# Performance work log

Hardware: AMD Instinct MI355X
Metric: run time of the kernel (lower is better)

The kernel has to match this reference:

```python
import jax, jax.numpy as jnp
import numpy as np

N, L = 64, 128
D = (32, 16, 8)   # input mode dims
H = (32, 16, 8)   # hidden mode dims


def setup_inputs() -> dict:
    key = jax.random.key(0)
    ks = jax.random.split(key, 7)
    inputs = jax.random.normal(ks[0], (N, L, *D), dtype=jnp.float32)
    # 3 gates (z, r, h) stacked along leading axis g; one factor matrix per mode.
    W1 = jax.random.normal(ks[1], (3, H[0], D[0]), dtype=jnp.float32) * 0.1
    W2 = jax.random.normal(ks[2], (3, H[1], D[1]), dtype=jnp.float32) * 0.1
    W3 = jax.random.normal(ks[3], (3, H[2], D[2]), dtype=jnp.float32) * 0.1
    U1 = jax.random.normal(ks[4], (3, H[0], H[0]), dtype=jnp.float32) * 0.1
    U2 = jax.random.normal(ks[5], (3, H[1], H[1]), dtype=jnp.float32) * 0.1
    U3 = jax.random.normal(ks[6], (3, H[2], H[2]), dtype=jnp.float32) * 0.1
    return {"inputs": inputs, "W1": W1, "W2": W2, "W3": W3,
            "U1": U1, "U2": U2, "U3": U3}


def reference(inputs, W1, W2, W3, U1, U2, U3):
    # batch_first -> (L, N, a, b, c)
    x = jnp.transpose(inputs, (1, 0, 2, 3, 4))
    # Precompute input projections for all timesteps and all 3 gates at once
    # (same math as applying TCL per step; mode-wise tensor contraction).
    XW = jnp.einsum('lnabc,gda,geb,gfc->lgndef', x, W1, W2, W3)  # (L,3,N,h1,h2,h3)
    h0 = jnp.zeros((x.shape[1], U1.shape[1], U2.shape[1], U3.shape[1]), x.dtype)

    def step(h, xw):
        hu = jnp.einsum('nabc,gda,geb,gfc->gndef', h, U1, U2, U3)  # (3,N,h1,h2,h3)
        z = jax.nn.sigmoid(xw[0] + hu[0])
        r = jax.nn.sigmoid(xw[1] + hu[1])
        hh = jnp.tanh(xw[2] + r * hu[2])
        h_new = z * h + (1.0 - z) * hh
        return h_new, h_new

    h_last, outs = jax.lax.scan(step, h0, XW)          # outs: (L,N,h1,h2,h3)
    outs = jnp.transpose(outs, (1, 0, 2, 3, 4))         # back to batch_first
    return outs, h_last
```

## Files before the change

### kernel.cpp

```cpp
#include <hip/hip_runtime.h>
#include <stdint.h>


constexpr int kN = 64;
constexpr int kL = 128;
constexpr int kA = 32, kB = 16, kC = 8;
constexpr int kBC = kB * kC;
constexpr int kTot = kA * kBC;
constexpr int kTS = kBC + 4;
constexpr int kTh = 512;
constexpr int kXwTiles = 8;

constexpr int kHTS = 40;
constexpr int kT1S = 136;

typedef __attribute__((ext_vector_type(8))) short bf16x8;
typedef __attribute__((ext_vector_type(4))) float f32x4;

namespace {

__device__ __forceinline__ float bf2f(unsigned int u) { return __uint_as_float(u << 16); }
__device__ __forceinline__ unsigned int f2bf(float v) {
  unsigned int u = __float_as_uint(v);
  return (u + 0x7fffu + ((u >> 16) & 1u)) >> 16;
}
__device__ __forceinline__ float sigmoid_f(float x) {
  return __fdividef(1.f, 1.f + __expf(-x));
}
__device__ __forceinline__ float tanh_f(float x) {
  return 1.f - __fdividef(2.f, 1.f + __expf(2.f * x));
}

__device__ __forceinline__ bf16x8 frag_from_lds(const unsigned short* p) {
  uint4 u = *(const uint4*)p;
  return __builtin_bit_cast(bf16x8, u);
}
__device__ __forceinline__ bf16x8 frag_from_f32(const float* p) {
  float4 a = ((const float4*)p)[0];
  float4 b = ((const float4*)p)[1];
  uint4 u;
  u.x = f2bf(a.x) | (f2bf(a.y) << 16);
  u.y = f2bf(a.z) | (f2bf(a.w) << 16);
  u.z = f2bf(b.x) | (f2bf(b.y) << 16);
  u.w = f2bf(b.z) | (f2bf(b.w) << 16);
  return __builtin_bit_cast(bf16x8, u);
}
__device__ __forceinline__ uint2 pack4(const f32x4& a) {
  uint2 p;
  p.x = f2bf(a[0]) | (f2bf(a[1]) << 16);
  p.y = f2bf(a[2]) | (f2bf(a[3]) << 16);
  return p;
}

__global__ void kron_kernel(const float* __restrict__ W2, const float* __restrict__ W3,
                            const float* __restrict__ U2, const float* __restrict__ U3,
                            unsigned short* __restrict__ kW, unsigned short* __restrict__ kU) {
  int i = blockIdx.x * 256 + threadIdx.x;
  const float* M2 = W2; const float* M3 = W3; unsigned short* dst = kW;
  int j = i;
  if (i >= 3 * 128 * 128) { M2 = U2; M3 = U3; dst = kU; j = i - 3 * 128 * 128; }
  int g = j >> 14, ef = (j >> 7) & 127, bc = j & 127;
  int e = ef >> 3, f = ef & 7, b = bc >> 3, c = bc & 7;
  float v = M2[(g * 16 + e) * 16 + b] * M3[(g * 8 + f) * 8 + c];
  dst[j] = (unsigned short)f2bf(v);
}

__device__ __forceinline__ void gemm1(const unsigned short* __restrict__ srcT,
                                      const bf16x8 bW[3][2],
                                      unsigned short (*__restrict__ t1L)[kA * kT1S],
                                      int w, int q, int r) {
  bf16x8 ah = frag_from_lds(srcT + (w * 16 + r) * kHTS + q * 8);
#pragma unroll
  for (int g = 0; g < 3; ++g) {
#pragma unroll
    for (int nt = 0; nt < 2; ++nt) {
      f32x4 acc = {0.f, 0.f, 0.f, 0.f};
      acc = __builtin_amdgcn_mfma_f32_16x16x32_bf16(ah, bW[g][nt], acc, 0, 0, 0);
      *(uint2*)&t1L[g][(nt * 16 + r) * kT1S + w * 16 + q * 4] = pack4(acc);
    }
  }
}

__device__ __forceinline__ void gemm2_scan(const unsigned short (*__restrict__ t1L)[kA * kT1S],
                                           const bf16x8 bK[3][2][4],
                                           f32x4 out2[3][2],
                                           int mtw, int q, int r) {
  const int abase = (mtw * 16 + r) * kT1S + q * 8;
#pragma unroll
  for (int g = 0; g < 3; ++g) {
    bf16x8 af[4];
#pragma unroll
    for (int kc = 0; kc < 4; ++kc)
      af[kc] = frag_from_lds(&t1L[g][abase + kc * 32]);
#pragma unroll
    for (int eft = 0; eft < 2; ++eft) {
      f32x4 acc = {0.f, 0.f, 0.f, 0.f};
#pragma unroll
      for (int kc = 0; kc < 4; ++kc)
        acc = __builtin_amdgcn_mfma_f32_16x16x32_bf16(af[kc], bK[g][eft][kc], acc, 0, 0, 0);
      out2[g][eft] = acc;
    }
  }
}

__device__ __forceinline__ void load_bfrags_scan(const unsigned short* __restrict__ kron,
                                                 const float* __restrict__ M1,
                                                 bf16x8 bK[3][2][4], bf16x8 bW[3][2],
                                                 int efb, int q, int r) {
#pragma unroll
  for (int g = 0; g < 3; ++g) {
#pragma unroll
    for (int eft = 0; eft < 2; ++eft)
#pragma unroll
      for (int kc = 0; kc < 4; ++kc)
        bK[g][eft][kc] = frag_from_lds(
            kron + ((g * 128 + (efb + 4 * eft) * 16 + r) * 128 + kc * 32 + q * 8));
#pragma unroll
    for (int nt = 0; nt < 2; ++nt)
      bW[g][nt] = frag_from_f32(M1 + (g * 32 + nt * 16 + r) * 32 + q * 8);
  }
}

__global__ __launch_bounds__(kTh) void xw_mfma(
    const float* __restrict__ x, const float* __restrict__ W1,
    const unsigned short* __restrict__ kW, unsigned short* __restrict__ xw) {
  __shared__ __align__(16) unsigned short xT[kBC * kHTS];
  __shared__ __align__(16) unsigned short t1L[3][kA * kT1S];
  const int tid = threadIdx.x;
  const int w = tid >> 6, l = tid & 63, q = l >> 4, r = l & 15;

  bf16x8 bK[3][4], bW[3][2];
#pragma unroll
  for (int g = 0; g < 3; ++g) {
#pragma unroll
    for (int kc = 0; kc < 4; ++kc)
      bK[g][kc] = frag_from_lds(kW + ((g * 128 + w * 16 + r) * 128 + kc * 32 + q * 8));
#pragma unroll
    for (int nt = 0; nt < 2; ++nt)
      bW[g][nt] = frag_from_f32(W1 + (g * 32 + nt * 16 + r) * 32 + q * 8);
  }

  const int bc = tid & 127, a0 = (tid >> 7) * 8;
  const int eftOfs = (w >> 2) * 4;

  for (int tt = 0; tt < kXwTiles; ++tt) {
    const int blk = blockIdx.x * kXwTiles + tt;

    {
      const float* xg = x + (size_t)blk * kTot + bc;
      uint4 u;
      u.x = f2bf(xg[(a0 + 0) * kBC]) | (f2bf(xg[(a0 + 1) * kBC]) << 16);
      u.y = f2bf(xg[(a0 + 2) * kBC]) | (f2bf(xg[(a0 + 3) * kBC]) << 16);
      u.z = f2bf(xg[(a0 + 4) * kBC]) | (f2bf(xg[(a0 + 5) * kBC]) << 16);
      u.w = f2bf(xg[(a0 + 6) * kBC]) | (f2bf(xg[(a0 + 7) * kBC]) << 16);
      *(uint4*)&xT[bc * kHTS + a0] = u;
    }
    __syncthreads();
    gemm1(xT, bW, t1L, w, q, r);
    __syncthreads();
    f32x4 out2[3][2];
#pragma unroll
    for (int g = 0; g < 3; ++g) {
#pragma unroll
      for (int mt = 0; mt < 2; ++mt) {
        f32x4 acc = {0.f, 0.f, 0.f, 0.f};
#pragma unroll
        for (int kc = 0; kc < 4; ++kc) {
          bf16x8 af = frag_from_lds(&t1L[g][(mt * 16 + r) * kT1S + kc * 32 + q * 8]);
          acc = __builtin_amdgcn_mfma_f32_16x16x32_bf16(af, bK[g][kc], acc, 0, 0, 0);
        }
        out2[g][mt] = acc;
      }
    }
#pragma unroll
    for (int g = 0; g < 3; ++g) {
      unsigned short* xo = xw + ((size_t)blk * 3 + g) * kTot;
#pragma unroll
      for (int mt = 0; mt < 2; ++mt) {
        const int wp = ((w & 3) << 1) | mt;
        uint2 p = pack4(out2[g][mt]);
        *(uint2*)(xo + (wp * 64 + q * 16 + r) * 8 + eftOfs) = p;
      }
    }
    __syncthreads();
  }
}

__global__ __launch_bounds__(kTh) void scan_mfma(
    const unsigned short* __restrict__ xw, const float* __restrict__ U1,
    const unsigned short* __restrict__ kU,
    float* __restrict__ outs, float* __restrict__ hlast) {
  __shared__ __align__(16) unsigned short hT[kBC * kHTS];
  __shared__ __align__(16) unsigned short t1L[3][kA * kT1S];
  const int tid = threadIdx.x;
  const int n = blockIdx.x;
  const int w = tid >> 6, l = tid & 63, q = l >> 4, r = l & 15;
  const int mtw = w & 1, efb = w >> 1;
  const int dbase = mtw * 16 + q * 4;

  bf16x8 bK[3][2][4], bW[3][2];
  load_bfrags_scan(kU, U1, bK, bW, efb, q, r);

  for (int i = tid; i < kBC * kHTS / 2; i += kTh) ((unsigned int*)hT)[i] = 0u;
  float hreg[2][4] = {{0.f, 0.f, 0.f, 0.f}, {0.f, 0.f, 0.f, 0.f}};

  const unsigned short* xp = xw + (size_t)n * kL * 3 * kTot + tid * 8;
  unsigned int xc[3][4];
#pragma unroll
  for (int g = 0; g < 3; ++g) {
    uint4 u = *(const uint4*)(xp + g * kTot);
    xc[g][0] = u.x; xc[g][1] = u.y; xc[g][2] = u.z; xc[g][3] = u.w;
  }
  __syncthreads();

  for (int t = 0; t < kL; ++t) {
    unsigned int xn[3][4];
    {
      const unsigned short* xq = xp + (size_t)((t + 1 < kL) ? t + 1 : t) * 3 * kTot;
#pragma unroll
      for (int g = 0; g < 3; ++g) {
        uint4 u = *(const uint4*)(xq + g * kTot);
        xn[g][0] = u.x; xn[g][1] = u.y; xn[g][2] = u.z; xn[g][3] = u.w;
      }
    }
    gemm1(hT, bW, t1L, w, q, r);
    __syncthreads();
    f32x4 hu[3][2];
    gemm2_scan(t1L, bK, hu, mtw, q, r);

    const size_t obase = ((size_t)n * kL + t) * kTot;
#pragma unroll
    for (int eft = 0; eft < 2; ++eft) {
      const int ef = (efb + 4 * eft) * 16 + r;
#pragma unroll
      for (int i = 0; i < 4; ++i) {
        const int e2 = eft * 4 + i;
        float x0 = bf2f((e2 & 1) ? (xc[0][e2 >> 1] >> 16) : (xc[0][e2 >> 1] & 0xffffu));
        float x1 = bf2f((e2 & 1) ? (xc[1][e2 >> 1] >> 16) : (xc[1][e2 >> 1] & 0xffffu));
        float x2 = bf2f((e2 & 1) ? (xc[2][e2 >> 1] >> 16) : (xc[2][e2 >> 1] & 0xffffu));
        float z  = sigmoid_f(x0 + hu[0][eft][i]);
        float rr = sigmoid_f(x1 + hu[1][eft][i]);
        float hc = tanh_f(x2 + rr * hu[2][eft][i]);
        float hn = z * hreg[eft][i] + (1.f - z) * hc;
        hreg[eft][i] = hn;
        outs[obase + (size_t)(dbase + i) * kBC + ef] = hn;
      }
      uint2 p;
      p.x = f2bf(hreg[eft][0]) | (f2bf(hreg[eft][1]) << 16);
      p.y = f2bf(hreg[eft][2]) | (f2bf(hreg[eft][3]) << 16);
      *(uint2*)&hT[ef * kHTS + dbase] = p;
    }
#pragma unroll
    for (int g = 0; g < 3; ++g)
#pragma unroll
      for (int u = 0; u < 4; ++u) xc[g][u] = xn[g][u];
    __syncthreads();
  }
#pragma unroll
  for (int eft = 0; eft < 2; ++eft) {
    const int ef = (efb + 4 * eft) * 16 + r;
#pragma unroll
    for (int i = 0; i < 4; ++i)
      hlast[(size_t)n * kTot + (size_t)(dbase + i) * kBC + ef] = hreg[eft][i];
  }
}

__device__ __forceinline__ int rfl(int v) { return __builtin_amdgcn_readfirstlane(v); }

__device__ __forceinline__ void load8f(const float* p, float* v) {
  float4 a = ((const float4*)p)[0];
  float4 b = ((const float4*)p)[1];
  v[0]=a.x; v[1]=a.y; v[2]=a.z; v[3]=a.w;
  v[4]=b.x; v[5]=b.y; v[6]=b.z; v[7]=b.w;
}
__device__ __forceinline__ void store8f(float* p, const float* v) {
  ((float4*)p)[0] = make_float4(v[0],v[1],v[2],v[3]);
  ((float4*)p)[1] = make_float4(v[4],v[5],v[6],v[7]);
}

__device__ __forceinline__ void mode1(const float* __restrict__ src,
                                      const float* __restrict__ Wg,
                                      float* __restrict__ t1, int tid) {
  const int w = rfl(tid >> 6);
  const int lane = tid & 63;
  const int bc = ((w & 1) << 6) | lane;
  const int dq = (w >> 1) << 3;
  float xr[kA];
#pragma unroll
  for (int a = 0; a < kA; ++a) xr[a] = src[a * kBC + bc];
  const float* wp = Wg + dq * kA;
#pragma unroll
  for (int dd = 0; dd < 8; ++dd) {
    float s = 0.f;
#pragma unroll
    for (int a = 0; a < kA; ++a) s += wp[dd * kA + a] * xr[a];
    t1[(dq + dd) * kTS + bc] = s;
  }
}
__device__ __forceinline__ void mode2(const float* __restrict__ t1,
                                      const float* __restrict__ Wg,
                                      float* __restrict__ t2, int tid) {
  const int w = rfl(tid >> 6);
  const int lane = tid & 63;
  const int d = ((w >> 1) << 3) | (lane >> 3);
  const int c = lane & 7;
  const int eh = (w & 1) << 3;
  float tr[kB];
#pragma unroll
  for (int b = 0; b < kB; ++b) tr[b] = t1[d * kTS + b * kC + c];
#pragma unroll
  for (int ee = 0; ee < 8; ++ee) {
    const int e = eh + ee;
    float s = 0.f;
#pragma unroll
    for (int b = 0; b < kB; ++b) s += Wg[e * kB + b] * tr[b];
    t2[d * kTS + e * kC + c] = s;
  }
}
__device__ __forceinline__ void mode3(const float* __restrict__ t2,
                                      const float* __restrict__ Wg,
                                      float* __restrict__ out8, int tid) {
  const int e = tid & 15;
  const int d = tid >> 4;
  float tr[kC];
  load8f(t2 + d * kTS + e * kC, tr);
#pragma unroll
  for (int f = 0; f < kC; ++f) {
    float s = 0.f;
#pragma unroll
    for (int c = 0; c < kC; ++c) s += Wg[f * kC + c] * tr[c];
    out8[f] = s;
  }
}

__global__ __launch_bounds__(kTh) void fused_kernel(
    const float* __restrict__ x,
    const float* __restrict__ W1, const float* __restrict__ W2,
    const float* __restrict__ W3, const float* __restrict__ U1,
    const float* __restrict__ U2, const float* __restrict__ U3,
    float* __restrict__ outs, float* __restrict__ hlast) {
  __shared__ float h[kTot];
  __shared__ float xs[kTot];
  __shared__ float t1[kA * kTS];
  __shared__ float t2[kA * kTS];
  const int tid = threadIdx.x;
  const int n = blockIdx.x;
  for (int i = tid; i < kTot; i += kTh) h[i] = 0.f;
  const int off = tid * kC;
  float* hp = h + off;
  float hn[kC];
  for (int l = 0; l < kL; ++l) {
    const float4* xg = (const float4*)(x + ((size_t)n * kL + l) * kTot);
    float4 xa = xg[tid], xb = xg[tid + kTh];
    __syncthreads();
    float4* xs4 = (float4*)xs;
    xs4[tid] = xa;
    xs4[tid + kTh] = xb;
    __syncthreads();
    float xwv[3][kC], hu[3][kC];
#pragma unroll
    for (int g = 0; g < 3; ++g) {
      mode1(xs, W1 + g * kA * kA, t1, tid);
      __syncthreads();
      mode2(t1, W2 + g * kB * kB, t2, tid);
      __syncthreads();
      mode3(t2, W3 + g * kC * kC, xwv[g], tid);
    }
#pragma unroll
    for (int g = 0; g < 3; ++g) {
      mode1(h, U1 + g * kA * kA, t1, tid);
      __syncthreads();
      mode2(t1, U2 + g * kB * kB, t2, tid);
      __syncthreads();
      mode3(t2, U3 + g * kC * kC, hu[g], tid);
    }
    float ho[kC];
    load8f(hp, ho);
#pragma unroll
    for (int f = 0; f < kC; ++f) {
      float z  = sigmoid_f(xwv[0][f] + hu[0][f]);
      float rr = sigmoid_f(xwv[1][f] + hu[1][f]);
      float hh = tanh_f(xwv[2][f] + rr * hu[2][f]);
      hn[f] = z * ho[f] + (1.f - z) * hh;
    }
    store8f(hp, hn);
    store8f(outs + ((size_t)n * kL + l) * kTot + off, hn);
  }
  store8f(hlast + (size_t)n * kTot + off, hn);
}

}

extern "C" void kernel_launch(void* const* d_in, const int* in_sizes, int n_in,
                              void* d_out, int out_size, void* d_ws, size_t ws_size,
                              hipStream_t stream) {
  const float* x  = (const float*)d_in[0];
  const float* W1 = (const float*)d_in[1];
  const float* W2 = (const float*)d_in[2];
  const float* W3 = (const float*)d_in[3];
  const float* U1 = (const float*)d_in[4];
  const float* U2 = (const float*)d_in[5];
  const float* U3 = (const float*)d_in[6];
  float* outs  = (float*)d_out;
  float* hlast = outs + (size_t)kN * kL * kTot;

  const size_t kron_elems = 3 * 128 * 128;
  const size_t kron_bytes = 2 * kron_elems * sizeof(unsigned short);
  const size_t xw_bytes   = (size_t)kN * kL * 3 * kTot * 2;

  if (ws_size >= kron_bytes + xw_bytes) {
    unsigned short* kW  = (unsigned short*)d_ws;
    unsigned short* kU  = kW + kron_elems;
    unsigned short* xww = kU + kron_elems;
    kron_kernel<<<dim3(384), dim3(256), 0, stream>>>(W2, W3, U2, U3, kW, kU);
    xw_mfma<<<dim3(kN * kL / kXwTiles), dim3(kTh), 0, stream>>>(x, W1, kW, xww);
    scan_mfma<<<dim3(kN), dim3(kTh), 0, stream>>>(xww, U1, kU, outs, hlast);
  } else {
    fused_kernel<<<dim3(kN), dim3(kTh), 0, stream>>>(x, W1, W2, W3, U1, U2, U3,
                                                     outs, hlast);
  }
}
```

Baseline: 600.2 us.

## Double-buffer x tiles with register prefetch in xw_mfma and double tiles per block

The input-projection kernel now loads the next x tile into registers while the current tile runs through both GEMM stages, then writes it into the alternate half of a double-buffered LDS array at the end of the iteration. This removes one barrier per tile and hides global-load latency behind MFMA work. Tiles per block also go from 8 to 16, which halves the grid and amortises the per-block weight-fragment loads. The trade-offs are more LDS and registers, plus fewer blocks available to spread across CUs.

```diff
diff --git a/kernel.cpp b/kernel.cpp
--- a/kernel.cpp
+++ b/kernel.cpp
@@ -9,7 +9,7 @@
 constexpr int kTot = kA * kBC;
 constexpr int kTS = kBC + 4;
 constexpr int kTh = 512;
-constexpr int kXwTiles = 8;
+constexpr int kXwTiles = 16;
 
 constexpr int kHTS = 40;
 constexpr int kT1S = 136;
@@ -50,6 +50,14 @@
   p.x = f2bf(a[0]) | (f2bf(a[1]) << 16);
   p.y = f2bf(a[2]) | (f2bf(a[3]) << 16);
   return p;
+}
+__device__ __forceinline__ uint4 pack8(const float* v) {
+  uint4 u;
+  u.x = f2bf(v[0]) | (f2bf(v[1]) << 16);
+  u.y = f2bf(v[2]) | (f2bf(v[3]) << 16);
+  u.z = f2bf(v[4]) | (f2bf(v[5]) << 16);
+  u.w = f2bf(v[6]) | (f2bf(v[7]) << 16);
+  return u;
 }
 
 __global__ void kron_kernel(const float* __restrict__ W2, const float* __restrict__ W3,
@@ -124,7 +132,7 @@
 __global__ __launch_bounds__(kTh) void xw_mfma(
     const float* __restrict__ x, const float* __restrict__ W1,
     const unsigned short* __restrict__ kW, unsigned short* __restrict__ xw) {
-  __shared__ __align__(16) unsigned short xT[kBC * kHTS];
+  __shared__ __align__(16) unsigned short xT[2][kBC * kHTS];
   __shared__ __align__(16) unsigned short t1L[3][kA * kT1S];
   const int tid = threadIdx.x;
   const int w = tid >> 6, l = tid & 63, q = l >> 4, r = l & 15;
@@ -142,21 +150,26 @@
 
   const int bc = tid & 127, a0 = (tid >> 7) * 8;
   const int eftOfs = (w >> 2) * 4;
+  const int blk0 = blockIdx.x * kXwTiles;
+
+  float xr[8];
+  {
+    const float* xg = x + (size_t)blk0 * kTot + bc;
+#pragma unroll
+    for (int j = 0; j < 8; ++j) xr[j] = xg[(a0 + j) * kBC];
+    *(uint4*)&xT[0][bc * kHTS + a0] = pack8(xr);
+  }
+  __syncthreads();
 
   for (int tt = 0; tt < kXwTiles; ++tt) {
-    const int blk = blockIdx.x * kXwTiles + tt;
-
+    const int blk = blk0 + tt;
     {
-      const float* xg = x + (size_t)blk * kTot + bc;
-      uint4 u;
-      u.x = f2bf(xg[(a0 + 0) * kBC]) | (f2bf(xg[(a0 + 1) * kBC]) << 16);
-      u.y = f2bf(xg[(a0 + 2) * kBC]) | (f2bf(xg[(a0 + 3) * kBC]) << 16);
-      u.z = f2bf(xg[(a0 + 4) * kBC]) | (f2bf(xg[(a0 + 5) * kBC]) << 16);
-      u.w = f2bf(xg[(a0 + 6) * kBC]) | (f2bf(xg[(a0 + 7) * kBC]) << 16);
-      *(uint4*)&xT[bc * kHTS + a0] = u;
-    }
-    __syncthreads();
-    gemm1(xT, bW, t1L, w, q, r);
+      const int nx = (tt + 1 < kXwTiles) ? tt + 1 : tt;
+      const float* xg = x + (size_t)(blk0 + nx) * kTot + bc;
+#pragma unroll
+      for (int j = 0; j < 8; ++j) xr[j] = xg[(a0 + j) * kBC];
+    }
+    gemm1(xT[tt & 1], bW, t1L, w, q, r);
     __syncthreads();
     f32x4 out2[3][2];
 #pragma unroll
@@ -182,6 +195,7 @@
         *(uint2*)(xo + (wp * 64 + q * 16 + r) * 8 + eftOfs) = p;
       }
     }
+    *(uint4*)&xT[(tt + 1) & 1][bc * kHTS + a0] = pack8(xr);
     __syncthreads();
   }
 }
```

Measured after the change: 588.0 us. -2.0%, faster.
